# Optimization experiments

Hardware: AMD Instinct MI355X
Metric: run time of the kernel (lower is better)

Reference implementation:

```python
import jax, jax.numpy as jnp
import numpy as np

N_NODES = 50000
N_EDGES = 800000
D = 96
LN_EPS = 1e-5


def setup_inputs() -> dict:
    key = jax.random.key(0)
    ks = jax.random.split(key, 4)
    x = jax.random.normal(ks[0], (N_NODES, D), dtype=jnp.float32)
    edge_index = jax.random.randint(ks[1], (2, N_EDGES), 0, N_NODES, dtype=jnp.int64)
    scale = 1.0 / np.sqrt(D)
    W0 = jax.random.normal(ks[2], (D, D), dtype=jnp.float32) * scale
    W1 = jax.random.normal(ks[3], (D, D), dtype=jnp.float32) * scale
    b0 = jnp.zeros((D,), jnp.float32)
    b1 = jnp.zeros((D,), jnp.float32)
    g0 = jnp.ones((D,), jnp.float32)
    g1 = jnp.ones((D,), jnp.float32)
    be0 = jnp.zeros((D,), jnp.float32)
    be1 = jnp.zeros((D,), jnp.float32)
    return {"x": x, "edge_index": edge_index, "W0": W0, "b0": b0, "g0": g0,
            "be0": be0, "W1": W1, "b1": b1, "g1": g1, "be1": be1}


def _layer(h, src, dst, norm, n_nodes, W, b, g, be):
    # GCNConv: h' = scatter_add(norm * (h W)[src]) + b  (self-loops included in src/dst)
    h = h @ W                                  # [N, out]
    msg = h[src] * norm[:, None]               # [E+N, out] gather (memory-bound)
    h = jax.ops.segment_sum(msg, dst, num_segments=n_nodes) + b
    h = jnp.tanh(h)
    mu = jnp.mean(h, axis=-1, keepdims=True)
    var = jnp.mean(jnp.square(h - mu), axis=-1, keepdims=True)
    h = (h - mu) * jax.lax.rsqrt(var + LN_EPS)
    return h * g + be


def reference(x, edge_index, W0, b0, g0, be0, W1, b1, g1, be1):
    n = x.shape[0]
    loops = jnp.arange(n, dtype=edge_index.dtype)
    src = jnp.concatenate([edge_index[0], loops])  # add self-loops (PyG default)
    dst = jnp.concatenate([edge_index[1], loops])
    deg = jax.ops.segment_sum(jnp.ones(src.shape, x.dtype), dst, num_segments=n)
    dis = jax.lax.rsqrt(deg)                       # deg >= 1 due to self-loops
    norm = dis[src] * dis[dst]                     # symmetric normalization
    h = _layer(x, src, dst, norm, n, W0, b0, g0, be0)
    h = _layer(h, src, dst, norm, n, W1, b1, g1, be1)
    return h  # dropout is identity in eval mode
```

## Files before the change

### kernel.cpp

```cpp
#include <hip/hip_runtime.h>
#include <hip/hip_bf16.h>
#include <type_traits>

#define D 96
#define LN_EPS 1e-5f
#define CHUNK 1024
#define BCAP 8192
#define BCAPP (BCAP + 1792)

typedef unsigned short ushort_t;
typedef __attribute__((ext_vector_type(8))) short short8;
typedef __attribute__((ext_vector_type(4))) float f32x4;

__device__ __forceinline__ ushort_t f2bf(float f) {
    unsigned u = __float_as_uint(f);
    u += 0x7FFF + ((u >> 16) & 1);
    return (ushort_t)(u >> 16);
}
__device__ __forceinline__ float blo(unsigned v) {
    return __uint_as_float(v << 16);
}
__device__ __forceinline__ float bhi(unsigned v) {
    return __uint_as_float(v & 0xffff0000u);
}

__global__ __launch_bounds__(256) void k_init(const unsigned* __restrict__ w,
                                              int* __restrict__ flag,
                                              int* __restrict__ gcur,
                                              ushort_t* __restrict__ hs, int N,
                                              int nbuk,
                                              const float* __restrict__ W0,
                                              const float* __restrict__ W1,
                                              ushort_t* __restrict__ Wt0,
                                              ushort_t* __restrict__ Wt1) {
    int t = threadIdx.x;
    if (blockIdx.x == 0) {
        __shared__ int anynz;
        if (t == 0) anynz = 0;
        __syncthreads();
        if ((t & 1) && w[t] != 0) anynz = 1;
        if (t < nbuk) gcur[t] = t * BCAP;
        if (t < 48) ((unsigned*)hs)[(size_t)N * 48 + t] = 0;
        __syncthreads();
        if (t == 0) *flag = (anynz == 0) ? 1 : 0;
    } else {
        int idx = (blockIdx.x - 1) * 256 + t;
        int sel = idx / 9216, i = idx % 9216;
        int c = i / 96, k = i % 96;
        const float* W = sel ? W1 : W0;
        ushort_t* Wt = sel ? Wt1 : Wt0;
        Wt[c * 96 + k] = f2bf(W[k * 96 + c]);
    }
}

__device__ __forceinline__ int load_idx(const void* eb, int is64, long long pos) {
    if (is64) return (int)((const long long*)eb)[pos];
    return ((const int*)eb)[pos];
}

__global__ __launch_bounds__(256) void k_bfill(const void* __restrict__ eb,
                                               const int* __restrict__ flag,
                                               int* __restrict__ gcur,
                                               unsigned* __restrict__ part, int E) {
    __shared__ int hist[256];
    __shared__ int cur[256];
    int t = threadIdx.x;
    hist[t] = 0;
    __syncthreads();
    int is64 = *flag;
    long long base = (long long)blockIdx.x * CHUNK;
    int sv[CHUNK / 256];
    int dv[CHUNK / 256];
    #pragma unroll
    for (int i = 0; i < CHUNK / 256; ++i) {
        long long e = base + t + (long long)i * 256;
        if (e < E) {
            sv[i] = load_idx(eb, is64, e);
            dv[i] = load_idx(eb, is64, (long long)E + e);
            atomicAdd(&hist[dv[i] >> 8], 1);
        } else dv[i] = -1;
    }
    __syncthreads();
    if (hist[t] > 0) cur[t] = atomicAdd(&gcur[t], hist[t]);
    __syncthreads();
    #pragma unroll
    for (int i = 0; i < CHUNK / 256; ++i) {
        if (dv[i] >= 0) {
            int b = dv[i] >> 8;
            int pos = atomicAdd(&cur[b], 1);
            part[pos] = ((unsigned)sv[i] << 8) | (unsigned)(dv[i] & 255);
        }
    }
}

__global__ __launch_bounds__(256) void k_build(const unsigned* __restrict__ part,
                                               const int* __restrict__ gcur,
                                               int* __restrict__ rbeg,
                                               int* __restrict__ rend,
                                               int* __restrict__ csr_src,
                                               float* __restrict__ dis,
                                               int N) {
    __shared__ int bins[256];
    __shared__ int cur[256];
    __shared__ int sh[256];
    int t = threadIdx.x;
    int b = blockIdx.x;
    int beg = b * BCAP, end = gcur[b];
    bins[t] = 0;
    __syncthreads();
    for (int i = beg + t; i < end; i += 256)
        atomicAdd(&bins[part[i] & 255u], 1);
    __syncthreads();
    int deg = bins[t];
    int pdeg = (deg + 7) & ~7;
    sh[t] = pdeg;
    __syncthreads();
    for (int off = 1; off < 256; off <<= 1) {
        int x = (t >= off) ? sh[t - off] : 0;
        __syncthreads();
        sh[t] += x;
        __syncthreads();
    }
    int mybeg = b * BCAPP + (sh[t] - pdeg);
    int node = b * 256 + t;
    if (node < N) {
        rbeg[node] = mybeg;
        rend[node] = mybeg + pdeg;
        dis[node] = rsqrtf((float)(deg + 1));
    }
    cur[t] = mybeg;
    __syncthreads();
    for (int i = beg + t; i < end; i += 256) {
        unsigned p = part[i];
        int pos = atomicAdd(&cur[p & 255u], 1);
        csr_src[pos] = (int)(p >> 8);
    }
    for (int k = deg; k < pdeg; ++k) csr_src[mybeg + k] = N;
}

template<typename T>
__global__ __launch_bounds__(256) void k_gemm_mfma(const T* __restrict__ A,
                                                   const ushort_t* __restrict__ Wt,
                                                   const float* __restrict__ dis,
                                                   ushort_t* __restrict__ Hs, int N) {
    __shared__ ushort_t As[64][104];
    __shared__ ushort_t Bs[96][104];
    int t = threadIdx.x;
    int row0 = blockIdx.x * 64;

    if constexpr (std::is_same<T, float>::value) {
        const float4* X4 = (const float4*)A;
        #pragma unroll
        for (int i = 0; i < 6; ++i) {
            int idx = t + i * 256;
            int r = idx / 24, c4 = idx % 24;
            float4 v = make_float4(0.f, 0.f, 0.f, 0.f);
            if (row0 + r < N) v = X4[(size_t)(row0 + r) * 24 + c4];
            ushort4 o;
            o.x = f2bf(v.x); o.y = f2bf(v.y); o.z = f2bf(v.z); o.w = f2bf(v.w);
            *(ushort4*)&As[r][c4 * 4] = o;
        }
    } else {
        #pragma unroll
        for (int i = 0; i < 3; ++i) {
            int idx = t + i * 256;
            int r = idx / 12, c8 = idx % 12;
            short8 v = {0, 0, 0, 0, 0, 0, 0, 0};
            if (row0 + r < N) v = *(const short8*)(A + (size_t)(row0 + r) * 96 + c8 * 8);
            *(short8*)&As[r][c8 * 8] = v;
        }
    }
    #pragma unroll
    for (int i = 0; i < 5; ++i) {
        int idx = t + i * 256;
        if (idx < 1152) {
            int r = idx / 12, c8 = idx % 12;
            *(short8*)&Bs[r][c8 * 8] = *(const short8*)(Wt + r * 96 + c8 * 8);
        }
    }
    __syncthreads();

    int w = t >> 6, l = t & 63;
    int lr = l & 15, lq = l >> 4;
    f32x4 acc[6];
    #pragma unroll
    for (int c = 0; c < 6; ++c) acc[c] = (f32x4){0.f, 0.f, 0.f, 0.f};

    #pragma unroll
    for (int q = 0; q < 3; ++q) {
        short8 af = *(const short8*)&As[w * 16 + lr][q * 32 + lq * 8];
        #pragma unroll
        for (int c = 0; c < 6; ++c) {
            short8 bf = *(const short8*)&Bs[c * 16 + lr][q * 32 + lq * 8];
            acc[c] = __builtin_amdgcn_mfma_f32_16x16x32_bf16(af, bf, acc[c], 0, 0, 0);
        }
    }

    int rbase = row0 + w * 16 + lq * 4;
    #pragma unroll
    for (int r = 0; r < 4; ++r) {
        int gr = rbase + r;
        if (gr < N) {
            float dr = dis[gr];
            ushort_t* o = Hs + (size_t)gr * 96 + lr;
            #pragma unroll
            for (int c = 0; c < 6; ++c) o[c * 16] = f2bf(dr * acc[c][r]);
        }
    }
}

template<bool BF16OUT>
__global__ __launch_bounds__(256) void k_agg_ln(const ushort_t* __restrict__ hs,
                                                const int* __restrict__ rbeg,
                                                const int* __restrict__ rend,
                                                const int* __restrict__ csr_src,
                                                const float* __restrict__ dis,
                                                const float* __restrict__ b,
                                                const float* __restrict__ g,
                                                const float* __restrict__ be,
                                                void* __restrict__ outp, int N) {
    int node = blockIdx.x * 8 + (threadIdx.x >> 5);
    int lane = threadIdx.x & 31;
    if (node >= N) return;

    const unsigned* h32 = (const unsigned*)hs;
    float a0, a1, a2 = 0.f, a3 = 0.f;
    {
        unsigned v = h32[(size_t)node * 48 + lane];
        a0 = blo(v); a1 = bhi(v);
        if (lane < 16) {
            unsigned u = h32[(size_t)node * 48 + 32 + lane];
            a2 = blo(u); a3 = bhi(u);
        }
    }

    int beg = rbeg[node], end = rend[node];
    for (int cb = beg; cb < end; cb += 32) {
        int m = min(32, end - cb);
        int e = cb + lane;
        int sreg = (e < end) ? csr_src[e] : 0;
        for (int j = 0; j < m; j += 8) {
            int s0 = __shfl(sreg, j, 32);
            int s1 = __shfl(sreg, j + 1, 32);
            int s2 = __shfl(sreg, j + 2, 32);
            int s3 = __shfl(sreg, j + 3, 32);
            int s4 = __shfl(sreg, j + 4, 32);
            int s5 = __shfl(sreg, j + 5, 32);
            int s6 = __shfl(sreg, j + 6, 32);
            int s7 = __shfl(sreg, j + 7, 32);
            unsigned v0 = h32[s0 * 48 + lane];
            unsigned v1 = h32[s1 * 48 + lane];
            unsigned v2 = h32[s2 * 48 + lane];
            unsigned v3 = h32[s3 * 48 + lane];
            unsigned v4 = h32[s4 * 48 + lane];
            unsigned v5 = h32[s5 * 48 + lane];
            unsigned v6 = h32[s6 * 48 + lane];
            unsigned v7 = h32[s7 * 48 + lane];
            a0 += blo(v0) + blo(v1) + blo(v2) + blo(v3)
                + blo(v4) + blo(v5) + blo(v6) + blo(v7);
            a1 += bhi(v0) + bhi(v1) + bhi(v2) + bhi(v3)
                + bhi(v4) + bhi(v5) + bhi(v6) + bhi(v7);
            if (lane < 16) {
                unsigned w0 = h32[s0 * 48 + 32 + lane];
                unsigned w1 = h32[s1 * 48 + 32 + lane];
                unsigned w2 = h32[s2 * 48 + 32 + lane];
                unsigned w3 = h32[s3 * 48 + 32 + lane];
                unsigned w4 = h32[s4 * 48 + 32 + lane];
                unsigned w5 = h32[s5 * 48 + 32 + lane];
                unsigned w6 = h32[s6 * 48 + 32 + lane];
                unsigned w7 = h32[s7 * 48 + 32 + lane];
                a2 += blo(w0) + blo(w1) + blo(w2) + blo(w3)
                    + blo(w4) + blo(w5) + blo(w6) + blo(w7);
                a3 += bhi(w0) + bhi(w1) + bhi(w2) + bhi(w3)
                    + bhi(w4) + bhi(w5) + bhi(w6) + bhi(w7);
            }
        }
    }

    float dn = dis[node];
    float2 b01 = ((const float2*)b)[lane];
    a0 = tanhf(fmaf(dn, a0, b01.x));
    a1 = tanhf(fmaf(dn, a1, b01.y));
    float s1 = a0 + a1;
    float s2 = a0 * a0 + a1 * a1;
    if (lane < 16) {
        float2 b23 = ((const float2*)b)[32 + lane];
        a2 = tanhf(fmaf(dn, a2, b23.x));
        a3 = tanhf(fmaf(dn, a3, b23.y));
        s1 += a2 + a3;
        s2 += a2 * a2 + a3 * a3;
    }
    #pragma unroll
    for (int off = 16; off >= 1; off >>= 1) {
        s1 += __shfl_xor(s1, off, 32);
        s2 += __shfl_xor(s2, off, 32);
    }
    float mu = s1 * (1.f / 96.f);
    float var = s2 * (1.f / 96.f) - mu * mu;
    float inv = rsqrtf(var + LN_EPS);

    float2 g01 = ((const float2*)g)[lane];
    float2 e01 = ((const float2*)be)[lane];
    float r0 = (a0 - mu) * inv * g01.x + e01.x;
    float r1 = (a1 - mu) * inv * g01.y + e01.y;
    if (BF16OUT) {
        unsigned* o32 = (unsigned*)outp + (size_t)node * 48;
        o32[lane] = ((unsigned)f2bf(r1) << 16) | (unsigned)f2bf(r0);
        if (lane < 16) {
            float2 g23 = ((const float2*)g)[32 + lane];
            float2 e23 = ((const float2*)be)[32 + lane];
            float r2 = (a2 - mu) * inv * g23.x + e23.x;
            float r3 = (a3 - mu) * inv * g23.y + e23.y;
            o32[32 + lane] = ((unsigned)f2bf(r3) << 16) | (unsigned)f2bf(r2);
        }
    } else {
        float2* o2 = (float2*)((float*)outp + (size_t)node * D);
        o2[lane] = make_float2(r0, r1);
        if (lane < 16) {
            float2 g23 = ((const float2*)g)[32 + lane];
            float2 e23 = ((const float2*)be)[32 + lane];
            o2[32 + lane] = make_float2((a2 - mu) * inv * g23.x + e23.x,
                                        (a3 - mu) * inv * g23.y + e23.y);
        }
    }
}

extern "C" void kernel_launch(void* const* d_in, const int* in_sizes, int n_in,
                              void* d_out, int out_size, void* d_ws, size_t ws_size,
                              hipStream_t stream) {
    const float* x  = (const float*)d_in[0];
    const void*  eb = d_in[1];
    const float* W0 = (const float*)d_in[2];
    const float* b0 = (const float*)d_in[3];
    const float* g0 = (const float*)d_in[4];
    const float* be0 = (const float*)d_in[5];
    const float* W1 = (const float*)d_in[6];
    const float* b1 = (const float*)d_in[7];
    const float* g1 = (const float*)d_in[8];
    const float* be1 = (const float*)d_in[9];

    const int N = in_sizes[0] / D;
    const int E = in_sizes[1] / 2;
    const int NBUK = (N + 255) >> 8;
    const int NBLK = (E + CHUNK - 1) / CHUNK;

    auto al = [](size_t v) { return (v + 255) & ~(size_t)255; };
    char* w = (char*)d_ws;
    size_t off = 0;
    int* flag = (int*)(w + off);          off = al(off + 4);
    int* gcur = (int*)(w + off);          off = al(off + 256 * 4);
    int* rbeg = (int*)(w + off);          off = al(off + (size_t)N * 4);
    int* rend = (int*)(w + off);          off = al(off + (size_t)N * 4);
    float* dis = (float*)(w + off);       off = al(off + (size_t)N * 4);
    int* csr_src = (int*)(w + off);       off = al(off + ((size_t)NBUK * BCAPP + 64) * 4);
    unsigned* part = (unsigned*)(w + off); off = al(off + ((size_t)NBUK * BCAP + BCAP) * 4);
    ushort_t* hs = (ushort_t*)(w + off);  off = al(off + ((size_t)N + 1) * D * 2);
    ushort_t* h1b = (ushort_t*)(w + off); off = al(off + (size_t)N * D * 2);
    ushort_t* Wt0 = (ushort_t*)(w + off); off = al(off + 9216 * 2);
    ushort_t* Wt1 = (ushort_t*)(w + off); off = al(off + 9216 * 2);
    float* outf = (float*)d_out;

    const int nbG = (N + 63) / 64;
    const int nbA = (N + 7) / 8;

    k_init<<<73, 256, 0, stream>>>((const unsigned*)eb, flag, gcur, hs, N, NBUK,
                                   W0, W1, Wt0, Wt1);
    k_bfill<<<NBLK, 256, 0, stream>>>(eb, flag, gcur, part, E);
    k_build<<<NBUK, 256, 0, stream>>>(part, gcur, rbeg, rend, csr_src, dis, N);

    k_gemm_mfma<float><<<nbG, 256, 0, stream>>>(x, Wt0, dis, hs, N);
    k_agg_ln<true><<<nbA, 256, 0, stream>>>(hs, rbeg, rend, csr_src, dis,
                                            b0, g0, be0, (void*)h1b, N);
    k_gemm_mfma<ushort_t><<<nbG, 256, 0, stream>>>(h1b, Wt1, dis, hs, N);
    k_agg_ln<false><<<nbA, 256, 0, stream>>>(hs, rbeg, rend, csr_src, dis,
                                             b1, g1, be1, (void*)outf, N);
}
```

Measured before the change: 122.1 us.

## Split feature rows into 64+32 planes and balance gather across all lanes

Stores the bf16 hidden features as two separate planes (64 columns and 32 columns) instead of one 96-wide row. In the aggregation, all 32 lanes now take part in fetching the 32-column tail, each half-warp covering different neighbours, and the two halves are combined with a shuffle. Previously half the lanes sat idle for that part. The change also splits the shared-memory histograms in the bucket-fill and CSR-build kernels into two halves to reduce atomic contention, and packs the begin/end row offsets into one int2. The risk is that gathers now touch two separate arrays, so each neighbour costs more distinct cache lines and memory transactions.

After: 120.4 us. No clear change (-1.4%).

```diff
diff --git a/kernel.cpp b/kernel.cpp
--- a/kernel.cpp
+++ b/kernel.cpp
@@ -27,7 +27,8 @@
 __global__ __launch_bounds__(256) void k_init(const unsigned* __restrict__ w,
                                               int* __restrict__ flag,
                                               int* __restrict__ gcur,
-                                              ushort_t* __restrict__ hs, int N,
+                                              unsigned* __restrict__ hsA,
+                                              unsigned* __restrict__ hsB, int N,
                                               int nbuk,
                                               const float* __restrict__ W0,
                                               const float* __restrict__ W1,
@@ -40,7 +41,8 @@
         __syncthreads();
         if ((t & 1) && w[t] != 0) anynz = 1;
         if (t < nbuk) gcur[t] = t * BCAP;
-        if (t < 48) ((unsigned*)hs)[(size_t)N * 48 + t] = 0;
+        if (t < 32) hsA[(size_t)N * 32 + t] = 0;
+        if (t < 16) hsB[(size_t)N * 16 + t] = 0;
         __syncthreads();
         if (t == 0) *flag = (anynz == 0) ? 1 : 0;
     } else {
@@ -62,10 +64,11 @@
                                                const int* __restrict__ flag,
                                                int* __restrict__ gcur,
                                                unsigned* __restrict__ part, int E) {
-    __shared__ int hist[256];
-    __shared__ int cur[256];
+    __shared__ int hist[2][256];
+    __shared__ int cur[2][256];
     int t = threadIdx.x;
-    hist[t] = 0;
+    int half = t >> 7;
+    hist[0][t] = 0; hist[1][t] = 0;
     __syncthreads();
     int is64 = *flag;
     long long base = (long long)blockIdx.x * CHUNK;
@@ -77,17 +80,21 @@
         if (e < E) {
             sv[i] = load_idx(eb, is64, e);
             dv[i] = load_idx(eb, is64, (long long)E + e);
-            atomicAdd(&hist[dv[i] >> 8], 1);
+            atomicAdd(&hist[half][dv[i] >> 8], 1);
         } else dv[i] = -1;
     }
     __syncthreads();
-    if (hist[t] > 0) cur[t] = atomicAdd(&gcur[t], hist[t]);
+    int h0 = hist[0][t], tot = h0 + hist[1][t];
+    int b0 = 0;
+    if (tot > 0) b0 = atomicAdd(&gcur[t], tot);
+    cur[0][t] = b0;
+    cur[1][t] = b0 + h0;
     __syncthreads();
     #pragma unroll
     for (int i = 0; i < CHUNK / 256; ++i) {
         if (dv[i] >= 0) {
             int b = dv[i] >> 8;
-            int pos = atomicAdd(&cur[b], 1);
+            int pos = atomicAdd(&cur[half][b], 1);
             part[pos] = ((unsigned)sv[i] << 8) | (unsigned)(dv[i] & 255);
         }
     }
@@ -95,23 +102,24 @@
 
 __global__ __launch_bounds__(256) void k_build(const unsigned* __restrict__ part,
                                                const int* __restrict__ gcur,
-                                               int* __restrict__ rbeg,
-                                               int* __restrict__ rend,
+                                               int2* __restrict__ rr,
                                                int* __restrict__ csr_src,
                                                float* __restrict__ dis,
                                                int N) {
-    __shared__ int bins[256];
-    __shared__ int cur[256];
+    __shared__ int bins[2][256];
+    __shared__ int cur[2][256];
     __shared__ int sh[256];
     int t = threadIdx.x;
     int b = blockIdx.x;
+    int half = t >> 7;
     int beg = b * BCAP, end = gcur[b];
-    bins[t] = 0;
+    bins[0][t] = 0; bins[1][t] = 0;
     __syncthreads();
     for (int i = beg + t; i < end; i += 256)
-        atomicAdd(&bins[part[i] & 255u], 1);
-    __syncthreads();
-    int deg = bins[t];
+        atomicAdd(&bins[half][part[i] & 255u], 1);
+    __syncthreads();
+    int d0 = bins[0][t];
+    int deg = d0 + bins[1][t];
     int pdeg = (deg + 7) & ~7;
     sh[t] = pdeg;
     __syncthreads();
@@ -124,32 +132,34 @@
     int mybeg = b * BCAPP + (sh[t] - pdeg);
     int node = b * 256 + t;
     if (node < N) {
-        rbeg[node] = mybeg;
-        rend[node] = mybeg + pdeg;
+        rr[node] = make_int2(mybeg, mybeg + pdeg);
         dis[node] = rsqrtf((float)(deg + 1));
     }
-    cur[t] = mybeg;
+    cur[0][t] = mybeg;
+    cur[1][t] = mybeg + d0;
     __syncthreads();
     for (int i = beg + t; i < end; i += 256) {
         unsigned p = part[i];
-        int pos = atomicAdd(&cur[p & 255u], 1);
+        int pos = atomicAdd(&cur[half][p & 255u], 1);
         csr_src[pos] = (int)(p >> 8);
     }
     for (int k = deg; k < pdeg; ++k) csr_src[mybeg + k] = N;
 }
 
 template<typename T>
-__global__ __launch_bounds__(256) void k_gemm_mfma(const T* __restrict__ A,
+__global__ __launch_bounds__(256) void k_gemm_mfma(const T* __restrict__ A0,
+                                                   const T* __restrict__ A1,
                                                    const ushort_t* __restrict__ Wt,
                                                    const float* __restrict__ dis,
-                                                   ushort_t* __restrict__ Hs, int N) {
+                                                   ushort_t* __restrict__ HsA,
+                                                   ushort_t* __restrict__ HsB, int N) {
     __shared__ ushort_t As[64][104];
     __shared__ ushort_t Bs[96][104];
     int t = threadIdx.x;
     int row0 = blockIdx.x * 64;
 
     if constexpr (std::is_same<T, float>::value) {
-        const float4* X4 = (const float4*)A;
+        const float4* X4 = (const float4*)A0;
         #pragma unroll
         for (int i = 0; i < 6; ++i) {
             int idx = t + i * 256;
@@ -166,7 +176,10 @@
             int idx = t + i * 256;
             int r = idx / 12, c8 = idx % 12;
             short8 v = {0, 0, 0, 0, 0, 0, 0, 0};
-            if (row0 + r < N) v = *(const short8*)(A + (size_t)(row0 + r) * 96 + c8 * 8);
+            if (row0 + r < N) {
+                if (c8 < 8) v = *(const short8*)(A0 + (size_t)(row0 + r) * 64 + c8 * 8);
+                else        v = *(const short8*)(A1 + (size_t)(row0 + r) * 32 + (c8 - 8) * 8);
+            }
             *(short8*)&As[r][c8 * 8] = v;
         }
     }
@@ -202,43 +215,49 @@
         int gr = rbase + r;
         if (gr < N) {
             float dr = dis[gr];
-            ushort_t* o = Hs + (size_t)gr * 96 + lr;
+            ushort_t* oA = HsA + (size_t)gr * 64 + lr;
+            ushort_t* oB = HsB + (size_t)gr * 32 + lr;
             #pragma unroll
-            for (int c = 0; c < 6; ++c) o[c * 16] = f2bf(dr * acc[c][r]);
+            for (int c = 0; c < 4; ++c) oA[c * 16] = f2bf(dr * acc[c][r]);
+            #pragma unroll
+            for (int c = 4; c < 6; ++c) oB[(c - 4) * 16] = f2bf(dr * acc[c][r]);
         }
     }
 }
 
 template<bool BF16OUT>
-__global__ __launch_bounds__(256) void k_agg_ln(const ushort_t* __restrict__ hs,
-                                                const int* __restrict__ rbeg,
-                                                const int* __restrict__ rend,
+__global__ __launch_bounds__(256) void k_agg_ln(const unsigned* __restrict__ hA32,
+                                                const unsigned* __restrict__ hB32,
+                                                const int2* __restrict__ rr,
                                                 const int* __restrict__ csr_src,
                                                 const float* __restrict__ dis,
                                                 const float* __restrict__ b,
                                                 const float* __restrict__ g,
                                                 const float* __restrict__ be,
-                                                void* __restrict__ outp, int N) {
+                                                void* __restrict__ outA,
+                                                void* __restrict__ outB, int N) {
     int node = blockIdx.x * 8 + (threadIdx.x >> 5);
     int lane = threadIdx.x & 31;
     if (node >= N) return;
 
-    const unsigned* h32 = (const unsigned*)hs;
-    float a0, a1, a2 = 0.f, a3 = 0.f;
+    float a0, a1, c0 = 0.f, c1 = 0.f;
     {
-        unsigned v = h32[(size_t)node * 48 + lane];
+        unsigned v = hA32[(size_t)node * 32 + lane];
         a0 = blo(v); a1 = bhi(v);
         if (lane < 16) {
-            unsigned u = h32[(size_t)node * 48 + 32 + lane];
-            a2 = blo(u); a3 = bhi(u);
-        }
-    }
-
-    int beg = rbeg[node], end = rend[node];
+            unsigned u = hB32[(size_t)node * 16 + lane];
+            c0 = blo(u); c1 = bhi(u);
+        }
+    }
+
+    int2 r = rr[node];
+    int beg = r.x, end = r.y;
+    int lsel = lane >> 4;
+    int lb = lane & 15;
     for (int cb = beg; cb < end; cb += 32) {
         int m = min(32, end - cb);
         int e = cb + lane;
-        int sreg = (e < end) ? csr_src[e] : 0;
+        int sreg = (e < end) ? csr_src[e] : (int)N;
         for (int j = 0; j < m; j += 8) {
             int s0 = __shfl(sreg, j, 32);
             int s1 = __shfl(sreg, j + 1, 32);
@@ -248,34 +267,33 @@
             int s5 = __shfl(sreg, j + 5, 32);
             int s6 = __shfl(sreg, j + 6, 32);
             int s7 = __shfl(sreg, j + 7, 32);
-            unsigned v0 = h32[s0 * 48 + lane];
-            unsigned v1 = h32[s1 * 48 + lane];
-            unsigned v2 = h32[s2 * 48 + lane];
-            unsigned v3 = h32[s3 * 48 + lane];
-            unsigned v4 = h32[s4 * 48 + lane];
-            unsigned v5 = h32[s5 * 48 + lane];
-            unsigned v6 = h32[s6 * 48 + lane];
-            unsigned v7 = h32[s7 * 48 + lane];
+            int p0 = __shfl(sreg, j + lsel, 32);
+            int p1 = __shfl(sreg, j + 2 + lsel, 32);
+            int p2 = __shfl(sreg, j + 4 + lsel, 32);
+            int p3 = __shfl(sreg, j + 6 + lsel, 32);
+            unsigned v0 = hA32[s0 * 32 + lane];
+            unsigned v1 = hA32[s1 * 32 + lane];
+            unsigned v2 = hA32[s2 * 32 + lane];
+            unsigned v3 = hA32[s3 * 32 + lane];
+            unsigned v4 = hA32[s4 * 32 + lane];
+            unsigned v5 = hA32[s5 * 32 + lane];
+            unsigned v6 = hA32[s6 * 32 + lane];
+            unsigned v7 = hA32[s7 * 32 + lane];
+            unsigned w0 = hB32[p0 * 16 + lb];
+            unsigned w1 = hB32[p1 * 16 + lb];
+            unsigned w2 = hB32[p2 * 16 + lb];
+            unsigned w3 = hB32[p3 * 16 + lb];
             a0 += blo(v0) + blo(v1) + blo(v2) + blo(v3)
                 + blo(v4) + blo(v5) + blo(v6) + blo(v7);
             a1 += bhi(v0) + bhi(v1) + bhi(v2) + bhi(v3)
                 + bhi(v4) + bhi(v5) + bhi(v6) + bhi(v7);
-            if (lane < 16) {
-                unsigned w0 = h32[s0 * 48 + 32 + lane];
-                unsigned w1 = h32[s1 * 48 + 32 + lane];
-                unsigned w2 = h32[s2 * 48 + 32 + lane];
-                unsigned w3 = h32[s3 * 48 + 32 + lane];
-                unsigned w4 = h32[s4 * 48 + 32 + lane];
-                unsigned w5 = h32[s5 * 48 + 32 + lane];
-                unsigned w6 = h32[s6 * 48 + 32 + lane];
-                unsigned w7 = h32[s7 * 48 + 32 + lane];
-                a2 += blo(w0) + blo(w1) + blo(w2) + blo(w3)
-                    + blo(w4) + blo(w5) + blo(w6) + blo(w7);
-                a3 += bhi(w0) + bhi(w1) + bhi(w2) + bhi(w3)
-                    + bhi(w4) + bhi(w5) + bhi(w6) + bhi(w7);
-            }
-        }
-    }
+            c0 += blo(w0) + blo(w1) + blo(w2) + blo(w3);
+            c1 += bhi(w0) + bhi(w1) + bhi(w2) + bhi(w3);
+        }
+    }
+
+    c0 += __shfl_xor(c0, 16, 32);
+    c1 += __shfl_xor(c1, 16, 32);
 
     float dn = dis[node];
     float2 b01 = ((const float2*)b)[lane];
@@ -283,10 +301,11 @@
     a1 = tanhf(fmaf(dn, a1, b01.y));
     float s1 = a0 + a1;
     float s2 = a0 * a0 + a1 * a1;
+    float a2 = 0.f, a3 = 0.f;
     if (lane < 16) {
         float2 b23 = ((const float2*)b)[32 + lane];
-        a2 = tanhf(fmaf(dn, a2, b23.x));
-        a3 = tanhf(fmaf(dn, a3, b23.y));
+        a2 = tanhf(fmaf(dn, c0, b23.x));
+        a3 = tanhf(fmaf(dn, c1, b23.y));
         s1 += a2 + a3;
         s2 += a2 * a2 + a3 * a3;
     }
@@ -304,17 +323,18 @@
     float r0 = (a0 - mu) * inv * g01.x + e01.x;
     float r1 = (a1 - mu) * inv * g01.y + e01.y;
     if (BF16OUT) {
-        unsigned* o32 = (unsigned*)outp + (size_t)node * 48;
-        o32[lane] = ((unsigned)f2bf(r1) << 16) | (unsigned)f2bf(r0);
+        ((unsigned*)outA)[(size_t)node * 32 + lane] =
+            ((unsigned)f2bf(r1) << 16) | (unsigned)f2bf(r0);
         if (lane < 16) {
             float2 g23 = ((const float2*)g)[32 + lane];
             float2 e23 = ((const float2*)be)[32 + lane];
             float r2 = (a2 - mu) * inv * g23.x + e23.x;
             float r3 = (a3 - mu) * inv * g23.y + e23.y;
-            o32[32 + lane] = ((unsigned)f2bf(r3) << 16) | (unsigned)f2bf(r2);
+            ((unsigned*)outB)[(size_t)node * 16 + lane] =
+                ((unsigned)f2bf(r3) << 16) | (unsigned)f2bf(r2);
         }
     } else {
-        float2* o2 = (float2*)((float*)outp + (size_t)node * D);
+        float2* o2 = (float2*)((float*)outA + (size_t)node * D);
         o2[lane] = make_float2(r0, r1);
         if (lane < 16) {
             float2 g23 = ((const float2*)g)[32 + lane];
@@ -349,13 +369,14 @@
     size_t off = 0;
     int* flag = (int*)(w + off);          off = al(off + 4);
     int* gcur = (int*)(w + off);          off = al(off + 256 * 4);
-    int* rbeg = (int*)(w + off);          off = al(off + (size_t)N * 4);
-    int* rend = (int*)(w + off);          off = al(off + (size_t)N * 4);
+    int2* rr = (int2*)(w + off);          off = al(off + (size_t)N * 8);
     float* dis = (float*)(w + off);       off = al(off + (size_t)N * 4);
     int* csr_src = (int*)(w + off);       off = al(off + ((size_t)NBUK * BCAPP + 64) * 4);
     unsigned* part = (unsigned*)(w + off); off = al(off + ((size_t)NBUK * BCAP + BCAP) * 4);
-    ushort_t* hs = (ushort_t*)(w + off);  off = al(off + ((size_t)N + 1) * D * 2);
-    ushort_t* h1b = (ushort_t*)(w + off); off = al(off + (size_t)N * D * 2);
+    unsigned* hsA = (unsigned*)(w + off); off = al(off + ((size_t)N + 1) * 128);
+    unsigned* hsB = (unsigned*)(w + off); off = al(off + ((size_t)N + 1) * 64);
+    ushort_t* h1A = (ushort_t*)(w + off); off = al(off + (size_t)N * 128);
+    ushort_t* h1B = (ushort_t*)(w + off); off = al(off + (size_t)N * 64);
     ushort_t* Wt0 = (ushort_t*)(w + off); off = al(off + 9216 * 2);
     ushort_t* Wt1 = (ushort_t*)(w + off); off = al(off + 9216 * 2);
     float* outf = (float*)d_out;
@@ -363,15 +384,17 @@
     const int nbG = (N + 63) / 64;
     const int nbA = (N + 7) / 8;
 
-    k_init<<<73, 256, 0, stream>>>((const unsigned*)eb, flag, gcur, hs, N, NBUK,
-                                   W0, W1, Wt0, Wt1);
+    k_init<<<73, 256, 0, stream>>>((const unsigned*)eb, flag, gcur, hsA, hsB, N,
+                                   NBUK, W0, W1, Wt0, Wt1);
     k_bfill<<<NBLK, 256, 0, stream>>>(eb, flag, gcur, part, E);
-    k_build<<<NBUK, 256, 0, stream>>>(part, gcur, rbeg, rend, csr_src, dis, N);
-
-    k_gemm_mfma<float><<<nbG, 256, 0, stream>>>(x, Wt0, dis, hs, N);
-    k_agg_ln<true><<<nbA, 256, 0, stream>>>(hs, rbeg, rend, csr_src, dis,
-                                            b0, g0, be0, (void*)h1b, N);
-    k_gemm_mfma<ushort_t><<<nbG, 256, 0, stream>>>(h1b, Wt1, dis, hs, N);
-    k_agg_ln<false><<<nbA, 256, 0, stream>>>(hs, rbeg, rend, csr_src, dis,
-                                             b1, g1, be1, (void*)outf, N);
-}
+    k_build<<<NBUK, 256, 0, stream>>>(part, gcur, rr, csr_src, dis, N);
+
+    k_gemm_mfma<float><<<nbG, 256, 0, stream>>>(x, (const float*)nullptr, Wt0, dis,
+                                                (ushort_t*)hsA, (ushort_t*)hsB, N);
+    k_agg_ln<true><<<nbA, 256, 0, stream>>>(hsA, hsB, rr, csr_src, dis,
+                                            b0, g0, be0, (void*)h1A, (void*)h1B, N);
+    k_gemm_mfma<ushort_t><<<nbG, 256, 0, stream>>>(h1A, h1B, Wt1, dis,
+                                                   (ushort_t*)hsA, (ushort_t*)hsB, N);
+    k_agg_ln<false><<<nbA, 256, 0, stream>>>(hsA, hsB, rr, csr_src, dis,
+                                             b1, g1, be1, (void*)outf, nullptr, N);
+}
```
